# Kernel optimization log

Measured on AMD Instinct MI355X. Metric: run time of the kernel, lower is better.

The kernel has to match this reference:

```python
import jax, jax.numpy as jnp
import numpy as np

B, C, H, W = 64, 64, 32, 32
K = 1024  # codebook_num
EPS = 1e-10


def setup_inputs() -> dict:
    key = jax.random.key(0)
    kz, kc = jax.random.split(key)
    z = jax.random.normal(kz, (B, C, H, W), dtype=jnp.float32)
    # nn.init.uniform_(codebook.weight, -1/K, 1/K)
    codebook = jax.random.uniform(kc, (K, C), dtype=jnp.float32, minval=-1.0 / K, maxval=1.0 / K)
    return {"z": z, "codebook": codebook}


def reference(z, codebook):
    Bz, Cz, Hz, Wz = z.shape
    flat_z = jnp.transpose(z, (0, 2, 3, 1)).reshape(-1, Cz)  # [N, C]
    dists = (jnp.sum(flat_z ** 2, axis=1, keepdims=True)
             + jnp.sum(codebook ** 2, axis=1)
             - 2.0 * flat_z @ codebook.T)
    indices = jnp.argmin(dists, axis=1)  # [N] int
    quantized_z = codebook[indices].reshape(Bz, Hz, Wz, Cz).transpose(0, 3, 1, 2)
    quantized_z_st = z + jax.lax.stop_gradient(quantized_z - z)
    # perplexity: probs = mean one-hot = histogram / N
    n = indices.shape[0]
    counts = jax.ops.segment_sum(jnp.ones((n,), dtype=jnp.float32), indices, num_segments=K)
    probs = counts / n
    perplexity = jnp.exp(-jnp.sum(probs * jnp.log(jnp.clip(probs, EPS))))
    return quantized_z, quantized_z_st, indices, perplexity
```

## Files before the change

kernel.cpp:

```cpp
#include <hip/hip_runtime.h>
#include <math.h>

#define NVEC   65536
#define CDIM   64
#define KBOOK  1024
#define NTOT   4194304


typedef _Float16 f16x8 __attribute__((ext_vector_type(8)));
typedef float    f32x4 __attribute__((ext_vector_type(4)));

__global__ void prep_kernel(const float* __restrict__ cb, float* __restrict__ se,
                            int* __restrict__ hist, _Float16* __restrict__ cbT,
                            float* __restrict__ se16, float* __restrict__ semax4,
                            unsigned* __restrict__ wcount, float* __restrict__ cbt) {
    __shared__ float lmax[4];
    const int t = blockIdx.x * 256 + threadIdx.x;
    if (t == 0) *wcount = 0u;
    hist[t] = 0;
    const float* row = cb + t * CDIM;
    float r[8];
#pragma unroll
    for (int j = 0; j < 8; ++j) r[j] = __fmul_rn(row[j], row[j]);
#pragma unroll
    for (int i = 8; i < 64; i += 8)
#pragma unroll
        for (int j = 0; j < 8; ++j) r[j] = __fadd_rn(r[j], __fmul_rn(row[i + j], row[i + j]));
    const float sev = __fadd_rn(__fadd_rn(__fadd_rn(r[0], r[1]), __fadd_rn(r[2], r[3])),
                                __fadd_rn(__fadd_rn(r[4], r[5]), __fadd_rn(r[6], r[7])));
    se[t] = sev;
    se16[t] = sev * 16384.0f;
    float m = sev;
#pragma unroll
    for (int off = 32; off > 0; off >>= 1) m = fmaxf(m, __shfl_xor(m, off));
    if ((threadIdx.x & 63) == 0) lmax[threadIdx.x >> 6] = m;
    __syncthreads();
    if (threadIdx.x == 0)
        semax4[blockIdx.x] = fmaxf(fmaxf(lmax[0], lmax[1]), fmaxf(lmax[2], lmax[3]));
#pragma unroll
    for (int c = 0; c < 64; ++c) cbt[c * 1024 + t] = row[c];
    const int tt = t >> 4, la = t & 15;
    _Float16* tb = cbT + (size_t)tt * 1024;
#pragma unroll
    for (int g = 0; g < 4; ++g)
#pragma unroll
        for (int j = 0; j < 8; ++j) {
            const float e0 = row[8 * g + j] * 16384.0f;
            const float e1 = row[32 + 8 * g + j] * 16384.0f;
            const int lo8 = (g * 16 + la) * 8 + j;
            tb[lo8]       = (_Float16)e0;
            tb[512 + lo8] = (_Float16)e1;
        }
}

__launch_bounds__(256)
__attribute__((amdgpu_waves_per_eu(4, 8)))
__global__ void approx_kernel(const float* __restrict__ z, const _Float16* __restrict__ cbT,
                              const float* __restrict__ se16, const float* __restrict__ semax4,
                              unsigned* __restrict__ result, unsigned* __restrict__ wlist,
                              unsigned* __restrict__ wcount, float* __restrict__ outIdxF,
                              int* __restrict__ hist) {
    __shared__ unsigned m1[4][16], m2[4][16];
    const int tid = threadIdx.x;
    const int w = tid >> 6;
    const int l = tid & 63;
    const int la = l & 15;
    const int g  = l >> 4;
    const int pair = w >> 1;
    const int kh = w & 1;
    const int n = blockIdx.x * 32 + pair * 16 + la;
    const int b = n >> 10, hw = n & 1023;
    const float* zb = z + (size_t)b * (CDIM * 1024) + hw;

    f16x8 mh0, mh1;
    float psum = 0.0f;
#pragma unroll
    for (int j = 0; j < 8; ++j) {
        {   float zc = zb[(g * 8 + j) * 1024];
            mh0[j] = (_Float16)(-2.0f * zc);
            psum = fmaf(zc, zc, psum); }
        {   float zc = zb[(32 + g * 8 + j) * 1024];
            mh1[j] = (_Float16)(-2.0f * zc);
            psum = fmaf(zc, zc, psum); }
    }

    unsigned u1k = 0xFFFFFFFFu, u2k = 0xFFFFFFFFu;
    const int kv = g * 4;
    const _Float16* tbase = cbT + (size_t)l * 8;

#define DECL_SLOT(s) f16x8 ah0_##s, ah1_##s; f32x4 se_##s;
    DECL_SLOT(a) DECL_SLOT(b)
#undef DECL_SLOT

#define LOADT(s, ttv) { const int t_ = (ttv) & 63;                       \
        const _Float16* p_ = tbase + (size_t)t_ * 1024;                  \
        ah0_##s = *(const f16x8*)(p_);                                   \
        ah1_##s = *(const f16x8*)(p_ + 512);                             \
        se_##s  = *(const f32x4*)(se16 + t_ * 16 + kv); }

#define PINS(acc_, r_, k0_) {                                            \
        unsigned ub = __float_as_uint(acc_[r_]);                         \
        ub = ((int)ub < 0) ? ~ub : (ub | 0x80000000u);                   \
        const unsigned key = (ub & 0xFFFFFC00u) | (unsigned)((k0_) + kv + (r_)); \
        const unsigned mx = (u1k > key) ? u1k : key;                     \
        u1k = (u1k < key) ? u1k : key;                                   \
        u2k = (u2k < mx) ? u2k : mx; }

#define COMPT(s, ttv) { const int k0_ = (ttv) * 16;                      \
        f32x4 acc = se_##s;                                              \
        acc = __builtin_amdgcn_mfma_f32_16x16x32_f16(ah0_##s, mh0, acc, 0, 0, 0); \
        acc = __builtin_amdgcn_mfma_f32_16x16x32_f16(ah1_##s, mh1, acc, 0, 0, 0); \
        PINS(acc, 0, k0_) PINS(acc, 1, k0_) PINS(acc, 2, k0_) PINS(acc, 3, k0_) }

    const int t0 = kh * 32;
    LOADT(a, t0)
    for (int tt = t0; tt < t0 + 32; tt += 2) {
        LOADT(b, tt + 1)
        COMPT(a, tt)
        LOADT(a, tt + 2)
        COMPT(b, tt + 1)
    }
#undef LOADT
#undef PINS
#undef COMPT

#pragma unroll
    for (int off = 16; off <= 32; off <<= 1) {
        const unsigned p1 = __shfl_xor(u1k, off);
        const unsigned p2 = __shfl_xor(u2k, off);
        psum += __shfl_xor(psum, off);
        const unsigned mx = (u1k > p1) ? u1k : p1;
        u1k = (u1k < p1) ? u1k : p1;
        const unsigned mm = (u2k < p2) ? u2k : p2;
        u2k = (mm < mx) ? mm : mx;
    }

    if (l < 16) { m1[w][la] = u1k; m2[w][la] = u2k; }
    __syncthreads();

    if (kh == 0 && l < 16) {
        const unsigned o1 = m1[w + 1][la], o2 = m2[w + 1][la];
        const unsigned mx = (u1k > o1) ? u1k : o1;
        const unsigned u1 = (u1k < o1) ? u1k : o1;
        unsigned u2 = (u2k < o2) ? u2k : o2;
        u2 = (u2 < mx) ? u2 : mx;

        const float sx = psum;
        const float srt = sqrtf(fmaxf(fmaxf(semax4[0], semax4[1]),
                                      fmaxf(semax4[2], semax4[3]))) * 1.0001f;
        const float THR = 60.2f * sqrtf(sx) * srt + 1.97e-2f * sx + 0.165f;
        const unsigned x1 = u1 & 0xFFFFFC00u, x2 = u2 & 0xFFFFFC00u;
        const float f1 = __uint_as_float((x1 & 0x80000000u) ? (x1 & 0x7FFFFFFFu) : ~x1);
        const float f2 = __uint_as_float((x2 & 0x80000000u) ? (x2 & 0x7FFFFFFFu) : ~x2);
        const int k1 = (int)(u1 & 1023u);
        if (f2 - f1 > THR) {
            result[n] = (unsigned)k1;
            outIdxF[n] = (float)k1;
            atomicAdd(&hist[k1], 1);
        } else {
            const unsigned widx = atomicAdd(wcount, 1u);
            wlist[widx] = (unsigned)n;
        }
    }
}

__launch_bounds__(256)
__global__ void rescore2_kernel(const float* __restrict__ z, const float* __restrict__ cbt,
                                const float* __restrict__ se,
                                const unsigned* __restrict__ wlist,
                                const unsigned* __restrict__ wcount,
                                unsigned* __restrict__ result, int* __restrict__ hist,
                                float* __restrict__ outIdxF) {
    __shared__ float zxs[4][64];
    __shared__ float rres[4][8];
    __shared__ float sxs[4];
    __shared__ unsigned long long red[4][4];
    const int cnt = (int)*wcount;
    const int tid = threadIdx.x;
    const int wv = tid >> 6, l = tid & 63;

    for (int base = blockIdx.x * 4; base < cnt; base += gridDim.x * 4) {
        const int ns = tid >> 6, c = tid & 63;
        const int item = base + ns;
        const int n = (int)wlist[(item < cnt) ? item : base];
        {
            const int b = n >> 10, hw = n & 1023;
            const float zc = z[(size_t)b * (CDIM * 1024) + c * 1024 + hw];
            zxs[ns][c] = zc + zc;
        }
        __syncthreads();
        if (c < 8) {
            const float z0 = zxs[ns][c] * 0.5f;
            float rr = __fmul_rn(z0, z0);
            for (int i = c + 8; i < 64; i += 8) {
                const float zi = zxs[ns][i] * 0.5f;
                rr = __fadd_rn(rr, __fmul_rn(zi, zi));
            }
            rres[ns][c] = rr;
        }
        __syncthreads();
        if (c == 0) {
            const float* r = rres[ns];
            sxs[ns] = __fadd_rn(__fadd_rn(__fadd_rn(r[0], r[1]), __fadd_rn(r[2], r[3])),
                                __fadd_rn(__fadd_rn(r[4], r[5]), __fadd_rn(r[6], r[7])));
        }
        __syncthreads();

        unsigned long long best0 = ~0ull, best1 = ~0ull, best2 = ~0ull, best3 = ~0ull;
        for (int chunk = 0; chunk < 4; ++chunk) {
            const int k = (chunk << 8) + tid;
            float a0 = 0.f, a1 = 0.f, a2 = 0.f, a3 = 0.f;
#pragma unroll 2
            for (int c4 = 0; c4 < 16; ++c4) {
                const float e0 = cbt[(4 * c4 + 0) * 1024 + k];
                const float e1 = cbt[(4 * c4 + 1) * 1024 + k];
                const float e2 = cbt[(4 * c4 + 2) * 1024 + k];
                const float e3 = cbt[(4 * c4 + 3) * 1024 + k];
                const f32x4 z0 = *(const f32x4*)&zxs[0][4 * c4];
                const f32x4 z1 = *(const f32x4*)&zxs[1][4 * c4];
                const f32x4 z2 = *(const f32x4*)&zxs[2][4 * c4];
                const f32x4 z3 = *(const f32x4*)&zxs[3][4 * c4];
                a0 = fmaf(z0[0], e0, a0); a0 = fmaf(z0[1], e1, a0);
                a0 = fmaf(z0[2], e2, a0); a0 = fmaf(z0[3], e3, a0);
                a1 = fmaf(z1[0], e0, a1); a1 = fmaf(z1[1], e1, a1);
                a1 = fmaf(z1[2], e2, a1); a1 = fmaf(z1[3], e3, a1);
                a2 = fmaf(z2[0], e0, a2); a2 = fmaf(z2[1], e1, a2);
                a2 = fmaf(z2[2], e2, a2); a2 = fmaf(z2[3], e3, a2);
                a3 = fmaf(z3[0], e0, a3); a3 = fmaf(z3[1], e1, a3);
                a3 = fmaf(z3[2], e2, a3); a3 = fmaf(z3[3], e3, a3);
            }
            const float sek = se[k];
#define DKEY(ai, bi) { const float d_ = __fsub_rn(__fadd_rn(sxs[bi], sek), ai);    \
        unsigned ob = __float_as_uint(d_);                                         \
        ob = (ob & 0x80000000u) ? ~ob : (ob | 0x80000000u);                        \
        const unsigned long long key = ((unsigned long long)ob << 32) | (unsigned)k; \
        if (key < best##bi) best##bi = key; }
            DKEY(a0, 0) DKEY(a1, 1) DKEY(a2, 2) DKEY(a3, 3)
#undef DKEY
        }

#define WRED(bi) {                                                       \
        unsigned long long b_ = best##bi;                                \
        _Pragma("unroll")                                                \
        for (int off = 1; off <= 32; off <<= 1) {                        \
            const unsigned long long o = __shfl_xor(b_, off);            \
            if (o < b_) b_ = o;                                          \
        }                                                                \
        if (l == 0) red[wv][bi] = b_; }
        WRED(0) WRED(1) WRED(2) WRED(3)
#undef WRED
        __syncthreads();
        if (tid < 4 && base + tid < cnt) {
            unsigned long long bb = red[0][tid];
            if (red[1][tid] < bb) bb = red[1][tid];
            if (red[2][tid] < bb) bb = red[2][tid];
            if (red[3][tid] < bb) bb = red[3][tid];
            const int n2 = (int)wlist[base + tid];
            const int kb = (int)(bb & 0xFFFFFFFFull);
            result[n2] = (unsigned)kb;
            outIdxF[n2] = (float)kb;
            atomicAdd(&hist[kb], 1);
        }
        __syncthreads();
    }
}

__global__ void scatter_kernel(const float* __restrict__ z, const float* __restrict__ cb,
                               const unsigned* __restrict__ result,
                               const int* __restrict__ hist,
                               float* __restrict__ out) {
    const int o = (blockIdx.x * 256 + threadIdx.x) * 4;
    const int b = o >> 16, c = (o >> 10) & 63, hw = o & 1023;
    const int n = (b << 10) | hw;
    float q[4];
#pragma unroll
    for (int j = 0; j < 4; ++j) {
        const int k = (int)result[n + j];
        q[j] = cb[k * CDIM + c];
    }
    const float4 zv = *(const float4*)(z + o);
    *(float4*)(out + o) = make_float4(q[0], q[1], q[2], q[3]);
    float4 st;
    st.x = __fadd_rn(zv.x, __fsub_rn(q[0], zv.x));
    st.y = __fadd_rn(zv.y, __fsub_rn(q[1], zv.y));
    st.z = __fadd_rn(zv.z, __fsub_rn(q[2], zv.z));
    st.w = __fadd_rn(zv.w, __fsub_rn(q[3], zv.w));
    *(float4*)(out + NTOT + o) = st;

    if (blockIdx.x == 0) {
        __shared__ double partial[4];
        const int t = threadIdx.x;
        double term = 0.0;
#pragma unroll
        for (int j = 0; j < 4; ++j) {
            const int cnt = hist[t + 256 * j];
            if (cnt > 0) { const double p = (double)cnt / (double)NVEC; term += p * log(p); }
        }
        for (int off = 32; off > 0; off >>= 1) term += __shfl_down(term, off);
        if ((t & 63) == 0) partial[t >> 6] = term;
        __syncthreads();
        if (t == 0) {
            const double sm = partial[0] + partial[1] + partial[2] + partial[3];
            out[2 * NTOT + NVEC] = (float)exp(-sm);
        }
    }
}

extern "C" void kernel_launch(void* const* d_in, const int* in_sizes, int n_in,
                              void* d_out, int out_size, void* d_ws, size_t ws_size,
                              hipStream_t stream) {
    const float* z  = (const float*)d_in[0];
    const float* cb = (const float*)d_in[1];
    float* out = (float*)d_out;

    char* ws = (char*)d_ws;
    unsigned* result = (unsigned*)ws;
    float* se   = (float*)(ws + 524288);
    int*   hist = (int*)(ws + 528384);

    char* outB = (char*)d_out;
    _Float16* cbT   = (_Float16*)(outB + (1 << 20));
    unsigned* wcount = (unsigned*)(outB + 1572864);
    float*    semax4 = (float*)(outB + 1572864 + 16);
    float*    se16   = (float*)(outB + 1572864 + 4096);
    unsigned* wlist  = (unsigned*)(outB + (2 << 20));
    float*    cbt    = (float*)(outB + (2 << 20) + (512 << 10));

    float* outIdxF = out + 2 * NTOT;

    prep_kernel<<<4, 256, 0, stream>>>(cb, se, hist, cbT, se16, semax4, wcount, cbt);
    approx_kernel<<<NVEC / 32, 256, 0, stream>>>(z, cbT, se16, semax4, result, wlist,
                                                 wcount, outIdxF, hist);
    rescore2_kernel<<<1024, 256, 0, stream>>>(z, cbt, se, wlist, wcount, result,
                                              hist, outIdxF);
    scatter_kernel<<<NTOT / 1024, 256, 0, stream>>>(z, cb, result, hist, out);
}
```

Baseline: 188.4 us.

## Reuse each codebook tile across four vector groups per wave in approx kernel

```diff
diff --git a/kernel.cpp b/kernel.cpp
--- a/kernel.cpp
+++ b/kernel.cpp
@@ -9,6 +9,8 @@
 
 typedef _Float16 f16x8 __attribute__((ext_vector_type(8)));
 typedef float    f32x4 __attribute__((ext_vector_type(4)));
+
+#define FORP(M) M(0) M(1) M(2) M(3)
 
 __global__ void prep_kernel(const float* __restrict__ cb, float* __restrict__ se,
                             int* __restrict__ hist, _Float16* __restrict__ cbT,
@@ -54,37 +56,41 @@
 }
 
 __launch_bounds__(256)
-__attribute__((amdgpu_waves_per_eu(4, 8)))
+__attribute__((amdgpu_waves_per_eu(4, 4)))
 __global__ void approx_kernel(const float* __restrict__ z, const _Float16* __restrict__ cbT,
                               const float* __restrict__ se16, const float* __restrict__ semax4,
                               unsigned* __restrict__ result, unsigned* __restrict__ wlist,
                               unsigned* __restrict__ wcount, float* __restrict__ outIdxF,
                               int* __restrict__ hist) {
-    __shared__ unsigned m1[4][16], m2[4][16];
+    __shared__ unsigned m1[4][4][16], m2[4][4][16];
     const int tid = threadIdx.x;
     const int w = tid >> 6;
     const int l = tid & 63;
     const int la = l & 15;
     const int g  = l >> 4;
-    const int pair = w >> 1;
-    const int kh = w & 1;
-    const int n = blockIdx.x * 32 + pair * 16 + la;
-    const int b = n >> 10, hw = n & 1023;
-    const float* zb = z + (size_t)b * (CDIM * 1024) + hw;
-
-    f16x8 mh0, mh1;
-    float psum = 0.0f;
-#pragma unroll
-    for (int j = 0; j < 8; ++j) {
-        {   float zc = zb[(g * 8 + j) * 1024];
-            mh0[j] = (_Float16)(-2.0f * zc);
-            psum = fmaf(zc, zc, psum); }
-        {   float zc = zb[(32 + g * 8 + j) * 1024];
-            mh1[j] = (_Float16)(-2.0f * zc);
-            psum = fmaf(zc, zc, psum); }
-    }
-
-    unsigned u1k = 0xFFFFFFFFu, u2k = 0xFFFFFFFFu;
+    const int nbase = blockIdx.x * 64;
+
+#define ZPRE(p)                                                          \
+    f16x8 mh0_##p, mh1_##p; float psum_##p = 0.0f; {                     \
+        const int n_ = nbase + (p) * 16 + la;                            \
+        const int b_ = n_ >> 10, hw_ = n_ & 1023;                        \
+        const float* zb_ = z + (size_t)b_ * (CDIM * 1024) + hw_;         \
+        _Pragma("unroll")                                                \
+        for (int j = 0; j < 8; ++j) {                                    \
+            { float zc = zb_[(g * 8 + j) * 1024];                        \
+              mh0_##p[j] = (_Float16)(-2.0f * zc);                       \
+              psum_##p = fmaf(zc, zc, psum_##p); }                       \
+            { float zc = zb_[(32 + g * 8 + j) * 1024];                   \
+              mh1_##p[j] = (_Float16)(-2.0f * zc);                       \
+              psum_##p = fmaf(zc, zc, psum_##p); }                       \
+        } }
+    FORP(ZPRE)
+#undef ZPRE
+
+#define KINIT(p) unsigned u1k_##p = 0xFFFFFFFFu, u2k_##p = 0xFFFFFFFFu;
+    FORP(KINIT)
+#undef KINIT
+
     const int kv = g * 4;
     const _Float16* tbase = cbT + (size_t)l * 8;
 
@@ -98,54 +104,72 @@
         ah1_##s = *(const f16x8*)(p_ + 512);                             \
         se_##s  = *(const f32x4*)(se16 + t_ * 16 + kv); }
 
-#define PINS(acc_, r_, k0_) {                                            \
-        unsigned ub = __float_as_uint(acc_[r_]);                         \
-        ub = ((int)ub < 0) ? ~ub : (ub | 0x80000000u);                   \
-        const unsigned key = (ub & 0xFFFFFC00u) | (unsigned)((k0_) + kv + (r_)); \
-        const unsigned mx = (u1k > key) ? u1k : key;                     \
-        u1k = (u1k < key) ? u1k : key;                                   \
-        u2k = (u2k < mx) ? u2k : mx; }
-
-#define COMPT(s, ttv) { const int k0_ = (ttv) * 16;                      \
+#define COMP1(s, p, k0_) {                                               \
         f32x4 acc = se_##s;                                              \
-        acc = __builtin_amdgcn_mfma_f32_16x16x32_f16(ah0_##s, mh0, acc, 0, 0, 0); \
-        acc = __builtin_amdgcn_mfma_f32_16x16x32_f16(ah1_##s, mh1, acc, 0, 0, 0); \
-        PINS(acc, 0, k0_) PINS(acc, 1, k0_) PINS(acc, 2, k0_) PINS(acc, 3, k0_) }
-
-    const int t0 = kh * 32;
+        acc = __builtin_amdgcn_mfma_f32_16x16x32_f16(ah0_##s, mh0_##p, acc, 0, 0, 0); \
+        acc = __builtin_amdgcn_mfma_f32_16x16x32_f16(ah1_##s, mh1_##p, acc, 0, 0, 0); \
+        _Pragma("unroll")                                                \
+        for (int r_ = 0; r_ < 4; ++r_) {                                 \
+            unsigned ub = __float_as_uint(acc[r_]);                      \
+            ub = ((int)ub < 0) ? ~ub : (ub | 0x80000000u);               \
+            const unsigned key = (ub & 0xFFFFFC00u) | (unsigned)((k0_) + r_); \
+            const unsigned mx = (u1k_##p > key) ? u1k_##p : key;         \
+            u1k_##p = (u1k_##p < key) ? u1k_##p : key;                   \
+            u2k_##p = (u2k_##p < mx) ? u2k_##p : mx;                     \
+        } }
+
+#define COMPT(s, ttv) { const int k0_ = (ttv) * 16 + kv;                 \
+        COMP1(s, 0, k0_) COMP1(s, 1, k0_) COMP1(s, 2, k0_) COMP1(s, 3, k0_) }
+
+    const int t0 = w * 16;
     LOADT(a, t0)
-    for (int tt = t0; tt < t0 + 32; tt += 2) {
+    for (int tt = t0; tt < t0 + 16; tt += 2) {
         LOADT(b, tt + 1)
         COMPT(a, tt)
         LOADT(a, tt + 2)
         COMPT(b, tt + 1)
     }
 #undef LOADT
-#undef PINS
+#undef COMP1
 #undef COMPT
 
-#pragma unroll
-    for (int off = 16; off <= 32; off <<= 1) {
-        const unsigned p1 = __shfl_xor(u1k, off);
-        const unsigned p2 = __shfl_xor(u2k, off);
-        psum += __shfl_xor(psum, off);
-        const unsigned mx = (u1k > p1) ? u1k : p1;
-        u1k = (u1k < p1) ? u1k : p1;
-        const unsigned mm = (u2k < p2) ? u2k : p2;
-        u2k = (mm < mx) ? mm : mx;
-    }
-
-    if (l < 16) { m1[w][la] = u1k; m2[w][la] = u2k; }
+#define BFLY(p) {                                                        \
+        _Pragma("unroll")                                                \
+        for (int off = 16; off <= 32; off <<= 1) {                       \
+            const unsigned p1 = __shfl_xor(u1k_##p, off);                \
+            const unsigned p2 = __shfl_xor(u2k_##p, off);                \
+            psum_##p += __shfl_xor(psum_##p, off);                       \
+            const unsigned mx = (u1k_##p > p1) ? u1k_##p : p1;           \
+            u1k_##p = (u1k_##p < p1) ? u1k_##p : p1;                     \
+            const unsigned mm = (u2k_##p < p2) ? u2k_##p : p2;           \
+            u2k_##p = (mm < mx) ? mm : mx;                               \
+        } }
+    FORP(BFLY)
+#undef BFLY
+
+    if (l < 16) {
+#define STOREM(p) m1[w][p][l] = u1k_##p; m2[w][p][l] = u2k_##p;
+        FORP(STOREM)
+#undef STOREM
+    }
     __syncthreads();
 
-    if (kh == 0 && l < 16) {
-        const unsigned o1 = m1[w + 1][la], o2 = m2[w + 1][la];
-        const unsigned mx = (u1k > o1) ? u1k : o1;
-        const unsigned u1 = (u1k < o1) ? u1k : o1;
-        unsigned u2 = (u2k < o2) ? u2k : o2;
-        u2 = (u2 < mx) ? u2 : mx;
-
-        const float sx = psum;
+    if (tid < 64) {
+        const int p = tid >> 4, la2 = tid & 15;
+        float sx = psum_0;
+        if (p == 1) sx = psum_1;
+        else if (p == 2) sx = psum_2;
+        else if (p == 3) sx = psum_3;
+        unsigned u1 = m1[0][p][la2], u2 = m2[0][p][la2];
+#pragma unroll
+        for (int ww = 1; ww < 4; ++ww) {
+            const unsigned o1 = m1[ww][p][la2], o2 = m2[ww][p][la2];
+            const unsigned mx = (u1 > o1) ? u1 : o1;
+            u1 = (u1 < o1) ? u1 : o1;
+            unsigned t2 = (u2 < o2) ? u2 : o2;
+            u2 = (t2 < mx) ? t2 : mx;
+        }
+
         const float srt = sqrtf(fmaxf(fmaxf(semax4[0], semax4[1]),
                                       fmaxf(semax4[2], semax4[3]))) * 1.0001f;
         const float THR = 60.2f * sqrtf(sx) * srt + 1.97e-2f * sx + 0.165f;
@@ -153,6 +177,7 @@
         const float f1 = __uint_as_float((x1 & 0x80000000u) ? (x1 & 0x7FFFFFFFu) : ~x1);
         const float f2 = __uint_as_float((x2 & 0x80000000u) ? (x2 & 0x7FFFFFFFu) : ~x2);
         const int k1 = (int)(u1 & 1023u);
+        const int n = nbase + tid;
         if (f2 - f1 > THR) {
             result[n] = (unsigned)k1;
             outIdxF[n] = (float)k1;
@@ -329,7 +354,7 @@
     float* outIdxF = out + 2 * NTOT;
 
     prep_kernel<<<4, 256, 0, stream>>>(cb, se, hist, cbT, se16, semax4, wcount, cbt);
-    approx_kernel<<<NVEC / 32, 256, 0, stream>>>(z, cbT, se16, semax4, result, wlist,
+    approx_kernel<<<NVEC / 64, 256, 0, stream>>>(z, cbT, se16, semax4, result, wlist,
                                                  wcount, outIdxF, hist);
     rescore2_kernel<<<1024, 256, 0, stream>>>(z, cbt, se, wlist, wcount, result,
                                               hist, outIdxF);
```

Result: faster. 166.8 us (-11.4%).
